# Performance work log

Measured on AMD Instinct MI355X. Metric: run time of the kernel, lower is better.

## Reference

```python
import jax, jax.numpy as jnp
import numpy as np


def _sobel_kernels(dtype):
    # kornia sobel order=1, normalized: divide by sum(|k|)=8
    gx = jnp.array([[-1., 0., 1.], [-2., 0., 2.], [-1., 0., 1.]], dtype=dtype) / 8.0
    gy = gx.T
    return jnp.stack([gx, gy])[:, None]  # (2, 1, 3, 3) OIHW


def _spatial_gradient(x):
    # x: (b, c, h, w) -> gx, gy each (b, c, h, w)
    b, c, h, w = x.shape
    xp = jnp.pad(x.reshape(b * c, 1, h, w), ((0, 0), (0, 0), (1, 1), (1, 1)), mode='edge')
    k = _sobel_kernels(x.dtype)
    out = jax.lax.conv_general_dilated(
        xp, k, window_strides=(1, 1), padding='VALID',
        dimension_numbers=('NCHW', 'OIHW', 'NCHW'))  # (b*c, 2, h, w)
    out = out.reshape(b, c, 2, h, w)
    return out[:, :, 0], out[:, :, 1]


def setup_inputs() -> dict:
    key = jax.random.key(0)
    x = jax.random.normal(key, (16, 3, 512, 512), dtype=jnp.float32)
    return {"x": x}


def reference(x):
    b, c, h, w = x.shape
    gx, gy = _spatial_gradient(x)  # (b, c, h, w) each
    if c == 3:
        mag_c = jnp.sqrt(gx * gx + gy * gy + 1e-9)  # per-channel magnitude
        # first-occurrence argmax over channels matches torch .max(dim) tie-break
        idx = jnp.argmax(mag_c, axis=1)  # (b, h, w)
        gxs = jnp.take_along_axis(gx, idx[:, None], axis=1)[:, 0]  # (b, h, w)
        gys = jnp.take_along_axis(gy, idx[:, None], axis=1)[:, 0]
    else:
        gxs, gys = gx, gy
    magnitude = jnp.sqrt(gxs * gxs + gys * gys + 1e-9)
    # clipped_div(gx, gy, 10.0)
    y_tr = jnp.where(gys == 0.0, jnp.asarray(1e-9, gys.dtype), gys)
    angle = jnp.clip(gxs / y_tr, -10.0, 10.0)
    return magnitude, angle
```

## Files before the change

### kernel.cpp

```cpp
#include <hip/hip_runtime.h>
#include <stdint.h>


constexpr int Hc = 512;
constexpr int Wc = 512;
constexpr int Cc = 3;
constexpr int RT = 4;
constexpr int ITERS = 8;
constexpr int SLOTS = 3;
constexpr int TILE_F = Cc * RT * Wc;

__global__ __launch_bounds__(256, 1) void sobel_mag_angle_kernel(
    const float* __restrict__ x, float* __restrict__ out, int B) {
    __shared__ float lds[SLOTS * TILE_F];

    int bid = blockIdx.x;
    int b = bid >> 4;
    int bstart = (bid & 15) << 5;

    int t = threadIdx.x;
    int wave = t >> 6;
    int lane = t & 63;
    int w0 = lane << 3;
    bool l0 = (lane == 0), l63 = (lane == 63);

    const float* xb = x + (size_t)b * (Cc * Hc * Wc);

    auto stage = [&](int j) {
        int slot = j % SLOTS;
#pragma unroll
        for (int s2 = 0; s2 < 6; ++s2) {
            int s = wave * 6 + s2;
            int c = s >> 3;
            int k = (s >> 1) & 3;
            int half = s & 1;
            int g = bstart - 1 + (j << 2) + k;
            g = g < 0 ? 0 : (g > Hc - 1 ? Hc - 1 : g);
            const float* gp = xb + ((size_t)c * Hc + g) * Wc + half * 256 + lane * 4;
            float* lp = &lds[slot * TILE_F + (c * RT + k) * Wc + half * 256];
            __builtin_amdgcn_global_load_lds(
                (const __attribute__((address_space(1))) void*)gp,
                (__attribute__((address_space(3))) void*)lp, 16, 0, 0);
        }
    };

    stage(0);
    stage(1);

    size_t npix = (size_t)B * (Hc * Wc);

    for (int i = 0; i < ITERS; ++i) {
        stage(i + 2);
        asm volatile("s_waitcnt vmcnt(6)" ::: "memory");
        __builtin_amdgcn_s_barrier();
        __builtin_amdgcn_sched_barrier(0);

        int si = i % SLOTS, si1 = (i + 1) % SLOTS;
        float bm[8], bgx[8], bgy[8];
#pragma unroll
        for (int c = 0; c < Cc; ++c) {
            float row[3][10];
#pragma unroll
            for (int d = 0; d < 3; ++d) {
                int idx = wave + d;
                int slot = idx < 4 ? si : si1;
                int k = idx < 4 ? idx : idx - 4;
                const float* lrow = &lds[slot * TILE_F + (c * RT + k) * Wc];
                float4 A  = *(const float4*)(lrow + w0);
                float4 Bv = *(const float4*)(lrow + w0 + 4);
                float lh = __shfl_up(Bv.w, 1);  lh = l0 ? A.x : lh;
                float rh = __shfl_down(A.x, 1); rh = l63 ? Bv.w : rh;
                row[d][0] = lh;
                row[d][1] = A.x;  row[d][2] = A.y;  row[d][3] = A.z;  row[d][4] = A.w;
                row[d][5] = Bv.x; row[d][6] = Bv.y; row[d][7] = Bv.z; row[d][8] = Bv.w;
                row[d][9] = rh;
            }
#pragma unroll
            for (int ii = 0; ii < 8; ++ii) {
                float t0 = row[0][ii + 2] - row[0][ii];
                float t1 = row[1][ii + 2] - row[1][ii];
                float t2 = row[2][ii + 2] - row[2][ii];
                float gx = 0.125f * (t0 + t2) + 0.25f * t1;
                float u0 = row[2][ii]     - row[0][ii];
                float u1 = row[2][ii + 1] - row[0][ii + 1];
                float u2 = row[2][ii + 2] - row[0][ii + 2];
                float gy = 0.125f * (u0 + u2) + 0.25f * u1;
                float m = __builtin_amdgcn_sqrtf(gx * gx + gy * gy + 1e-9f);
                if (c == 0) {
                    bm[ii] = m; bgx[ii] = gx; bgy[ii] = gy;
                } else {
                    bool gt = m > bm[ii];
                    bm[ii]  = gt ? m  : bm[ii];
                    bgx[ii] = gt ? gx : bgx[ii];
                    bgy[ii] = gt ? gy : bgy[ii];
                }
            }
        }

        float mo[8], ao[8];
#pragma unroll
        for (int ii = 0; ii < 8; ++ii) {
            mo[ii] = bm[ii];
            float yt = (bgy[ii] == 0.0f) ? 1e-9f : bgy[ii];
            float a = bgx[ii] * __builtin_amdgcn_rcpf(yt);
            ao[ii] = fminf(fmaxf(a, -10.0f), 10.0f);
        }

        int g = bstart + (i << 2) + wave;
        size_t obase = ((size_t)b * Hc + g) * Wc;
        float* po = out + obase;
        *(float4*)(po + w0)            = make_float4(mo[0], mo[1], mo[2], mo[3]);
        *(float4*)(po + w0 + 4)        = make_float4(mo[4], mo[5], mo[6], mo[7]);
        *(float4*)(po + npix + w0)     = make_float4(ao[0], ao[1], ao[2], ao[3]);
        *(float4*)(po + npix + w0 + 4) = make_float4(ao[4], ao[5], ao[6], ao[7]);

        __builtin_amdgcn_sched_barrier(0);
        __builtin_amdgcn_s_barrier();
    }
}

extern "C" void kernel_launch(void* const* d_in, const int* in_sizes, int n_in,
                              void* d_out, int out_size, void* d_ws, size_t ws_size,
                              hipStream_t stream) {
    const float* x = (const float*)d_in[0];
    float* out = (float*)d_out;
    int B = in_sizes[0] / (Cc * Hc * Wc);
    int blocks = B * (Hc / (RT * ITERS));
    sobel_mag_angle_kernel<<<blocks, 256, 0, stream>>>(x, out, B);
}
```

Baseline: 103.2 us.

## Use 512-thread blocks with 10-row halo tiles and double buffering

Each block now runs 8 waves and every iteration handles 8 output rows per channel. It loads a 10-row haloed tile through a two-slot double buffer, replacing the three-slot ring of 4-row chunks. Re-staging the halo rows each iteration costs some redundant global loads. In return the barrier count per row drops, fewer waves idle, and the 2-blocks-per-CU launch bound is meant to raise occupancy. The wave-to-slot clamp (s>59) makes waves 7's extra loads duplicate the same row, and LDS use rises to about 120KB per block, which may limit residency to one block per CU.

```diff
diff --git a/kernel.cpp b/kernel.cpp
--- a/kernel.cpp
+++ b/kernel.cpp
@@ -5,14 +5,13 @@
 constexpr int Hc = 512;
 constexpr int Wc = 512;
 constexpr int Cc = 3;
-constexpr int RT = 4;
-constexpr int ITERS = 8;
-constexpr int SLOTS = 3;
-constexpr int TILE_F = Cc * RT * Wc;
+constexpr int TROWS = 10;
+constexpr int TILE_F = Cc * TROWS * Wc;
+constexpr int ITERS = 4;
 
-__global__ __launch_bounds__(256, 1) void sobel_mag_angle_kernel(
+__global__ __launch_bounds__(512, 2) void sobel_mag_angle_kernel(
     const float* __restrict__ x, float* __restrict__ out, int B) {
-    __shared__ float lds[SLOTS * TILE_F];
+    __shared__ float lds[2 * TILE_F];
 
     int bid = blockIdx.x;
     int b = bid >> 4;
@@ -27,17 +26,20 @@
     const float* xb = x + (size_t)b * (Cc * Hc * Wc);
 
     auto stage = [&](int j) {
-        int slot = j % SLOTS;
+        int slot = j & 1;
+        int g0 = bstart - 1 + (j << 3);
 #pragma unroll
-        for (int s2 = 0; s2 < 6; ++s2) {
-            int s = wave * 6 + s2;
-            int c = s >> 3;
-            int k = (s >> 1) & 3;
-            int half = s & 1;
-            int g = bstart - 1 + (j << 2) + k;
+        for (int s2 = 0; s2 < 8; ++s2) {
+            int s = wave * 8 + s2;
+            if (s > 59) s = 59;
+            int c = s / 20;
+            int rem = s - c * 20;
+            int k = rem >> 1;
+            int half = rem & 1;
+            int g = g0 + k;
             g = g < 0 ? 0 : (g > Hc - 1 ? Hc - 1 : g);
             const float* gp = xb + ((size_t)c * Hc + g) * Wc + half * 256 + lane * 4;
-            float* lp = &lds[slot * TILE_F + (c * RT + k) * Wc + half * 256];
+            float* lp = &lds[slot * TILE_F + (c * TROWS + k) * Wc + half * 256];
             __builtin_amdgcn_global_load_lds(
                 (const __attribute__((address_space(1))) void*)gp,
                 (__attribute__((address_space(3))) void*)lp, 16, 0, 0);
@@ -45,27 +47,28 @@
     };
 
     stage(0);
-    stage(1);
 
     size_t npix = (size_t)B * (Hc * Wc);
 
+#pragma unroll
     for (int i = 0; i < ITERS; ++i) {
-        stage(i + 2);
-        asm volatile("s_waitcnt vmcnt(6)" ::: "memory");
+        if (i < ITERS - 1) {
+            stage(i + 1);
+            asm volatile("s_waitcnt vmcnt(8)" ::: "memory");
+        } else {
+            asm volatile("s_waitcnt vmcnt(0)" ::: "memory");
+        }
         __builtin_amdgcn_s_barrier();
         __builtin_amdgcn_sched_barrier(0);
 
-        int si = i % SLOTS, si1 = (i + 1) % SLOTS;
+        int slot = i & 1;
         float bm[8], bgx[8], bgy[8];
 #pragma unroll
         for (int c = 0; c < Cc; ++c) {
             float row[3][10];
 #pragma unroll
             for (int d = 0; d < 3; ++d) {
-                int idx = wave + d;
-                int slot = idx < 4 ? si : si1;
-                int k = idx < 4 ? idx : idx - 4;
-                const float* lrow = &lds[slot * TILE_F + (c * RT + k) * Wc];
+                const float* lrow = &lds[slot * TILE_F + (c * TROWS + wave + d) * Wc];
                 float4 A  = *(const float4*)(lrow + w0);
                 float4 Bv = *(const float4*)(lrow + w0 + 4);
                 float lh = __shfl_up(Bv.w, 1);  lh = l0 ? A.x : lh;
@@ -106,7 +109,7 @@
             ao[ii] = fminf(fmaxf(a, -10.0f), 10.0f);
         }
 
-        int g = bstart + (i << 2) + wave;
+        int g = bstart + (i << 3) + wave;
         size_t obase = ((size_t)b * Hc + g) * Wc;
         float* po = out + obase;
         *(float4*)(po + w0)            = make_float4(mo[0], mo[1], mo[2], mo[3]);
@@ -125,6 +128,6 @@
     const float* x = (const float*)d_in[0];
     float* out = (float*)d_out;
     int B = in_sizes[0] / (Cc * Hc * Wc);
-    int blocks = B * (Hc / (RT * ITERS));
-    sobel_mag_angle_kernel<<<blocks, 256, 0, stream>>>(x, out, B);
+    int blocks = B * (Hc / 32);
+    sobel_mag_angle_kernel<<<blocks, 512, 0, stream>>>(x, out, B);
 }
```

After: 99.88 us. 1.03x faster.
